# Performance work log

Hardware: AMD Instinct MI355X
Metric: run time of the kernel (lower is better)

## Reference

```python
import jax, jax.numpy as jnp
import numpy as np

H = 16
D_MODEL = 1024
D_K = D_MODEL // H
B, S = 4, 2048


def setup_inputs() -> dict:
    key = jax.random.key(0)
    ks = jax.random.split(key, 12)
    scale = 1.0 / np.sqrt(D_MODEL)
    inp = {
        "query": jax.random.normal(ks[0], (B, S, D_MODEL), jnp.float32),
        "key_in": jax.random.normal(ks[1], (B, S, D_MODEL), jnp.float32),
        "value": jax.random.normal(ks[2], (B, S, D_MODEL), jnp.float32),
        "mask": jax.random.randint(ks[3], (B, 1, S, S), 0, 2, jnp.int32),
    }
    # 4 Linear(d_model, d_model) layers: Wq, Wk, Wv, Wo (+ biases)
    names = ["q", "k", "v", "o"]
    for i, n in enumerate(names):
        inp[f"W{n}"] = jax.random.normal(ks[4 + i], (D_MODEL, D_MODEL), jnp.float32) * scale
        inp[f"b{n}"] = jax.random.normal(ks[8 + i], (D_MODEL,), jnp.float32) * scale
    return inp


def reference(query, key_in, value, mask, Wq, bq, Wk, bk, Wv, bv, Wo, bo):
    # Linear projections then split heads: [B,S,D] -> [B,H,S,Dk]
    def proj(x, W, b):
        y = jnp.einsum("bsd,ed->bse", x, W) + b  # torch Linear: x @ W.T + b
        return y.reshape(B, S, H, D_K).transpose(0, 2, 1, 3)

    q = proj(query, Wq, bq)
    k = proj(key_in, Wk, bk)
    v = proj(value, Wv, bv)

    scores = jnp.einsum("bhqd,bhkd->bhqk", q, k) / jnp.sqrt(jnp.float32(D_K))
    scores = jnp.where(mask == 0, jnp.float32(-1e9), scores)
    p_attn = jax.nn.softmax(scores, axis=-1)
    # dropout is identity in eval mode
    x = jnp.einsum("bhqk,bhkd->bhqd", p_attn, v)
    x = x.transpose(0, 2, 1, 3).reshape(B, S, D_MODEL)
    return jnp.einsum("bsd,ed->bse", x, Wo) + bo
```

## Files before the change

kernel.cpp:

```cpp
#include <hip/hip_runtime.h>
#include <hip/hip_bf16.h>

typedef __bf16 bf16_t;
typedef __attribute__((ext_vector_type(8))) __bf16 bf16x8;
typedef __attribute__((ext_vector_type(4))) __bf16 bf16x4;
typedef __attribute__((ext_vector_type(4))) float f32x4;

#define GAS __attribute__((address_space(1)))
#define LAS __attribute__((address_space(3)))

__device__ __forceinline__ void async_copy16(const bf16_t* g, bf16_t* l) {
    __builtin_amdgcn_global_load_lds((const GAS void*)g, (LAS void*)l, 16, 0, 0);
}

__global__ __launch_bounds__(256) void convert_kernel(
    const float* __restrict__ src, bf16_t* __restrict__ dst, int n)
{
    int i = (blockIdx.x * 256 + threadIdx.x) * 8;
    if (i >= n) return;
    f32x4 f0 = *(const f32x4*)(src + i);
    f32x4 f1 = *(const f32x4*)(src + i + 4);
    bf16x8 v;
#pragma unroll
    for (int j = 0; j < 4; j++) { v[j] = (bf16_t)f0[j]; v[4 + j] = (bf16_t)f1[j]; }
    *(bf16x8*)&dst[i] = v;
}

__global__ __launch_bounds__(256) void pack_mask_kernel(
    const int* __restrict__ mask, unsigned long long* __restrict__ out)
{
    int i = blockIdx.x * 256 + threadIdx.x;
    unsigned long long bits = __ballot(mask[i] != 0);
    if ((threadIdx.x & 63) == 0) out[i >> 6] = bits;
}

template<int MODE>
__global__ __launch_bounds__(256, 2) void gemm_nt(
    const bf16_t* __restrict__ A, const bf16_t* __restrict__ W,
    const float* __restrict__ bias, void* __restrict__ out_)
{
    __shared__ __align__(16) bf16_t Als[128 * 32];
    __shared__ __align__(16) bf16_t Bls[128 * 32];

    const int tid  = threadIdx.x;
    const int wave = tid >> 6, lane = tid & 63;
    const int quad = lane >> 4, lq = lane & 15;
    const int wm = wave >> 1, wn = wave & 1;
    const int tm = blockIdx.x * 128, tn = blockIdx.y * 128;
    const int K = 1024;

    const bf16_t* gA0 = A + (size_t)(tm + wave * 32 + (lane >> 2)) * K + (lane & 3) * 8;
    const bf16_t* gA1 = gA0 + (size_t)16 * K;
    const bf16_t* gB0 = W + (size_t)(tn + wave * 32 + (lane >> 2)) * K + (lane & 3) * 8;
    const bf16_t* gB1 = gB0 + (size_t)16 * K;
    bf16_t* lA0 = &Als[(wave * 32) * 32];
    bf16_t* lA1 = &Als[(wave * 32 + 16) * 32];
    bf16_t* lB0 = &Bls[(wave * 32) * 32];
    bf16_t* lB1 = &Bls[(wave * 32 + 16) * 32];

    f32x4 acc[4][4] = {};

    for (int k0 = 0; k0 < K; k0 += 32) {
        __syncthreads();
        async_copy16(gA0, lA0);
        async_copy16(gA1, lA1);
        async_copy16(gB0, lB0);
        async_copy16(gB1, lB1);
        gA0 += 32; gA1 += 32; gB0 += 32; gB1 += 32;
        __syncthreads();

        bf16x8 af[4], bfr[4];
#pragma unroll
        for (int i = 0; i < 4; i++) {
            af[i]  = *(const bf16x8*)&Als[(wm * 64 + i * 16 + lq) * 32 + quad * 8];
            bfr[i] = *(const bf16x8*)&Bls[(wn * 64 + i * 16 + lq) * 32 + quad * 8];
        }
#pragma unroll
        for (int i = 0; i < 4; i++)
#pragma unroll
            for (int j = 0; j < 4; j++) {
                if (MODE == 2)
                    acc[i][j] = __builtin_amdgcn_mfma_f32_16x16x32_bf16(bfr[j], af[i], acc[i][j], 0, 0, 0);
                else
                    acc[i][j] = __builtin_amdgcn_mfma_f32_16x16x32_bf16(af[i], bfr[j], acc[i][j], 0, 0, 0);
            }
    }

    float* outf = (float*)out_;
    bf16_t* outb = (bf16_t*)out_;
#pragma unroll
    for (int i = 0; i < 4; i++)
#pragma unroll
        for (int j = 0; j < 4; j++)
#pragma unroll
            for (int r = 0; r < 4; r++) {
                float v = acc[i][j][r];
                if (MODE == 0) {
                    int row = tm + wm * 64 + i * 16 + quad * 4 + r;
                    int col = tn + wn * 64 + j * 16 + lq;
                    outf[(size_t)row * 1024 + col] = v + bias[col];
                } else if (MODE == 1) {
                    int row = tm + wm * 64 + i * 16 + quad * 4 + r;
                    int col = tn + wn * 64 + j * 16 + lq;
                    v += bias[col];
                    int b = row >> 11, s = row & 2047;
                    int h = col >> 6,  dk = col & 63;
                    outb[(((size_t)(b * 16 + h) * 2048 + s) << 6) + dk] = (bf16_t)v;
                } else {
                    int n = tn + wn * 64 + j * 16 + quad * 4 + r;
                    int m = tm + wm * 64 + i * 16 + lq;
                    v += bias[n];
                    int b = m >> 11, s = m & 2047;
                    int h = n >> 6,  dk = n & 63;
                    outb[((size_t)((b * 16 + h) * 64 + dk) << 11) + s] = (bf16_t)v;
                }
            }
}

#define LDK 72
#define LDV 40
#define LDP 40

__global__ __launch_bounds__(256, 2) void attn_kernel(
    const bf16_t* __restrict__ Q, const bf16_t* __restrict__ Kh,
    const bf16_t* __restrict__ Vt, const unsigned int* __restrict__ mp,
    bf16_t* __restrict__ X)
{
    __shared__ __align__(16) bf16_t Kls[32 * LDK];
    __shared__ __align__(16) bf16_t Vls[64 * LDV];
    __shared__ __align__(16) bf16_t Pls[4][16 * LDP];

    const int tid  = threadIdx.x;
    const int wave = tid >> 6, lane = tid & 63;
    const int quad = lane >> 4, lq = lane & 15;
    const int bh = blockIdx.y;
    const int b  = bh >> 4;
    const int qw = blockIdx.x * 64 + wave * 16;

    const bf16_t* qptr = Q + ((size_t)bh * 2048 + qw + lq) * 64 + quad * 8;
    bf16x8 qf0 = *(const bf16x8*)qptr;
    bf16x8 qf1 = *(const bf16x8*)(qptr + 32);

    f32x4 o[4] = {};
    float lsum = 0.f;

    const int kr = tid >> 3, kc = tid & 7;
    const int vr = tid >> 2, vc = tid & 3;
    const bf16_t* gK = Kh + ((size_t)bh * 2048 + kr) * 64 + kc * 8;
    const bf16_t* gV = Vt + ((size_t)bh * 64 + vr) * 2048 + vc * 8;

    const unsigned int* mrow = mp + ((size_t)(b << 11) + qw + lq) * 64;

    for (int kt = 0; kt < 64; kt++) {
        unsigned int w = mrow[kt];
        bf16x8 kstage = *(const bf16x8*)gK;
        bf16x8 vstage = *(const bf16x8*)gV;
        gK += 2048; gV += 32;

        __syncthreads();
        *(bf16x8*)&Kls[kr * LDK + kc * 8] = kstage;
        *(bf16x8*)&Vls[vr * LDV + vc * 8] = vstage;
        __syncthreads();

        bf16_t* pb = &Pls[wave][0];
        const unsigned int wq = w >> (quad * 4);
#pragma unroll
        for (int nt = 0; nt < 2; nt++) {
            const bf16_t* krow = &Kls[(nt * 16 + lq) * LDK];
            bf16x8 kf0 = *(const bf16x8*)(krow + quad * 8);
            bf16x8 kf1 = *(const bf16x8*)(krow + 32 + quad * 8);
            f32x4 z = {};
            z = __builtin_amdgcn_mfma_f32_16x16x32_bf16(kf0, qf0, z, 0, 0, 0);
            z = __builtin_amdgcn_mfma_f32_16x16x32_bf16(kf1, qf1, z, 0, 0, 0);
            bf16x4 pk;
#pragma unroll
            for (int r = 0; r < 4; r++) {
                float sv = ((wq >> (nt * 16 + r)) & 1) ? z[r] * 0.125f : -1e9f;
                float p = __expf(sv);
                lsum += p;
                pk[r] = (bf16_t)p;
            }
            *(bf16x4*)&pb[lq * LDP + nt * 16 + quad * 4] = pk;
        }

        bf16x8 pf = *(const bf16x8*)&pb[lq * LDP + quad * 8];
#pragma unroll
        for (int dt = 0; dt < 4; dt++) {
            bf16x8 vf = *(const bf16x8*)&Vls[(dt * 16 + lq) * LDV + quad * 8];
            o[dt] = __builtin_amdgcn_mfma_f32_16x16x32_bf16(pf, vf, o[dt], 0, 0, 0);
        }
    }

    lsum += __shfl_xor(lsum, 16);
    lsum += __shfl_xor(lsum, 32);
    float rl[4];
#pragma unroll
    for (int r = 0; r < 4; r++) {
        float lv = __shfl(lsum, quad * 4 + r);
        rl[r] = (lv > 0.f) ? 1.0f / lv : 0.f;
    }
    const int h = bh & 15;
#pragma unroll
    for (int dt = 0; dt < 4; dt++)
#pragma unroll
        for (int r = 0; r < 4; r++) {
            int qrow = qw + quad * 4 + r;
            X[((size_t)(b * 2048) + qrow) * 1024 + h * 64 + dt * 16 + lq] =
                (bf16_t)(o[dt][r] * rl[r]);
        }
}

extern "C" void kernel_launch(void* const* d_in, const int* in_sizes, int n_in,
                              void* d_out, int out_size, void* d_ws, size_t ws_size,
                              hipStream_t stream)
{
    const float* query  = (const float*)d_in[0];
    const float* key_in = (const float*)d_in[1];
    const float* value  = (const float*)d_in[2];
    const int*   mask   = (const int*)d_in[3];

    char* ws = (char*)d_ws;
    const size_t SZ  = (size_t)8192 * 1024 * 2;
    const size_t MPK = (size_t)2 * 1024 * 1024;
    const size_t WSZ = (size_t)1024 * 1024 * 2;
    bf16_t* C   = (bf16_t*)(ws);
    bf16_t* Qb  = (bf16_t*)(ws + SZ);
    bf16_t* Kb  = (bf16_t*)(ws + 2 * SZ);
    bf16_t* Vtb = (bf16_t*)(ws + 3 * SZ);
    unsigned long long* mpack = (unsigned long long*)(ws + 4 * SZ);
    bf16_t* Wc[4];
    for (int i = 0; i < 4; i++)
        Wc[i] = (bf16_t*)(ws + 4 * SZ + MPK + i * WSZ);

    const size_t NEED = 4 * SZ + MPK + 4 * WSZ;
    if (ws_size < NEED) return;

    const int NACT = 8192 * 1024;
    for (int i = 0; i < 4; i++)
        convert_kernel<<<512, 256, 0, stream>>>((const float*)d_in[4 + 2 * i],
                                                Wc[i], 1024 * 1024);
    pack_mask_kernel<<<65536, 256, 0, stream>>>(mask, mpack);

    dim3 gg(64, 8);
    convert_kernel<<<4096, 256, 0, stream>>>(query, C, NACT);
    gemm_nt<1><<<gg, 256, 0, stream>>>(C, Wc[0], (const float*)d_in[5], Qb);
    convert_kernel<<<4096, 256, 0, stream>>>(key_in, C, NACT);
    gemm_nt<1><<<gg, 256, 0, stream>>>(C, Wc[1], (const float*)d_in[7], Kb);
    convert_kernel<<<4096, 256, 0, stream>>>(value, C, NACT);
    gemm_nt<2><<<gg, 256, 0, stream>>>(C, Wc[2], (const float*)d_in[9], Vtb);

    attn_kernel<<<dim3(32, 64), 256, 0, stream>>>(Qb, Kb, Vtb,
                                                  (const unsigned int*)mpack, C);
    gemm_nt<0><<<gg, 256, 0, stream>>>(C, Wc[3], (const float*)d_in[11], d_out);
}
```

Baseline: 473.7 us.

## Fuse activation conversion into QKV GEMM, double-buffer GEMMs and attention

The separate fp32-to-bf16 conversion passes for the activations are removed. The batched QKV GEMM (grid z=3) now loads fp32 A directly and converts it in registers, and the four weight conversions are merged into one launch. Both GEMMs and the attention kernel gain double-buffered LDS with a single barrier per step, so global loads overlap compute. Attention also gives each wave 32 query rows to reuse K/V tiles, at the cost of more registers and LDS.

Result: no change. 477.5 us (+0.8%).

```diff
diff --git a/kernel.cpp b/kernel.cpp
--- a/kernel.cpp
+++ b/kernel.cpp
@@ -13,17 +13,20 @@
     __builtin_amdgcn_global_load_lds((const GAS void*)g, (LAS void*)l, 16, 0, 0);
 }
 
-__global__ __launch_bounds__(256) void convert_kernel(
-    const float* __restrict__ src, bf16_t* __restrict__ dst, int n)
-{
-    int i = (blockIdx.x * 256 + threadIdx.x) * 8;
-    if (i >= n) return;
+__global__ __launch_bounds__(256) void wconvert_kernel(
+    const float* __restrict__ w0, const float* __restrict__ w1,
+    const float* __restrict__ w2, const float* __restrict__ w3,
+    bf16_t* __restrict__ dst)
+{
+    int which = blockIdx.x >> 9;
+    const float* src = which == 0 ? w0 : which == 1 ? w1 : which == 2 ? w2 : w3;
+    int i = ((blockIdx.x & 511) * 256 + threadIdx.x) * 8;
     f32x4 f0 = *(const f32x4*)(src + i);
     f32x4 f1 = *(const f32x4*)(src + i + 4);
     bf16x8 v;
 #pragma unroll
     for (int j = 0; j < 4; j++) { v[j] = (bf16_t)f0[j]; v[4 + j] = (bf16_t)f1[j]; }
-    *(bf16x8*)&dst[i] = v;
+    *(bf16x8*)&dst[(size_t)which * 1048576 + i] = v;
 }
 
 __global__ __launch_bounds__(256) void pack_mask_kernel(
@@ -34,13 +37,21 @@
     if ((threadIdx.x & 63) == 0) out[i >> 6] = bits;
 }
 
-template<int MODE>
-__global__ __launch_bounds__(256, 2) void gemm_nt(
-    const bf16_t* __restrict__ A, const bf16_t* __restrict__ W,
-    const float* __restrict__ bias, void* __restrict__ out_)
-{
-    __shared__ __align__(16) bf16_t Als[128 * 32];
-    __shared__ __align__(16) bf16_t Bls[128 * 32];
+__global__ __launch_bounds__(256, 2) void qkv_gemm(
+    const float* __restrict__ Aq, const float* __restrict__ Ak,
+    const float* __restrict__ Av, const bf16_t* __restrict__ Wall,
+    const float* __restrict__ bq, const float* __restrict__ bk,
+    const float* __restrict__ bv,
+    bf16_t* __restrict__ Qb, bf16_t* __restrict__ Kb, bf16_t* __restrict__ Vtb)
+{
+    const int z = blockIdx.z;
+    const float*  A    = z == 0 ? Aq : z == 1 ? Ak : Av;
+    const bf16_t* W    = Wall + (size_t)z * 1048576;
+    const float*  bias = z == 0 ? bq : z == 1 ? bk : bv;
+    bf16_t*       out  = z == 0 ? Qb : z == 1 ? Kb : Vtb;
+
+    __shared__ __align__(16) bf16_t Ab[2][128 * 32];
+    __shared__ __align__(16) bf16_t Wb[2][128 * 32];
 
     const int tid  = threadIdx.x;
     const int wave = tid >> 6, lane = tid & 63;
@@ -49,45 +60,57 @@
     const int tm = blockIdx.x * 128, tn = blockIdx.y * 128;
     const int K = 1024;
 
-    const bf16_t* gA0 = A + (size_t)(tm + wave * 32 + (lane >> 2)) * K + (lane & 3) * 8;
-    const bf16_t* gA1 = gA0 + (size_t)16 * K;
-    const bf16_t* gB0 = W + (size_t)(tn + wave * 32 + (lane >> 2)) * K + (lane & 3) * 8;
-    const bf16_t* gB1 = gB0 + (size_t)16 * K;
-    bf16_t* lA0 = &Als[(wave * 32) * 32];
-    bf16_t* lA1 = &Als[(wave * 32 + 16) * 32];
-    bf16_t* lB0 = &Bls[(wave * 32) * 32];
-    bf16_t* lB1 = &Bls[(wave * 32 + 16) * 32];
+    const int r0f = tid >> 3, c0f = tid & 7;
+    const float* gA = A + (size_t)(tm + r0f) * K + c0f * 4;
+    const bf16_t* gW0 = W + (size_t)(tn + wave * 32 + (lane >> 2)) * K + (lane & 3) * 8;
+    const bf16_t* gW1 = gW0 + (size_t)16 * K;
+    const int wd0 = (wave * 32) * 32, wd1 = (wave * 32 + 16) * 32;
+
+    f32x4 areg[4];
+#define LOAD_A(k) { _Pragma("unroll") \
+    for (int i = 0; i < 4; i++) areg[i] = *(const f32x4*)(gA + (size_t)(32 * i) * K + (k)); }
+#define WRITE_A(buf) { _Pragma("unroll") \
+    for (int i = 0; i < 4; i++) { bf16x4 v_; _Pragma("unroll") \
+        for (int j = 0; j < 4; j++) v_[j] = (bf16_t)areg[i][j]; \
+        *(bf16x4*)&Ab[buf][(r0f + 32 * i) * 32 + c0f * 4] = v_; } }
+#define DMA_W(k, buf) { async_copy16(gW0 + (k), &Wb[buf][wd0]); \
+                        async_copy16(gW1 + (k), &Wb[buf][wd1]); }
 
     f32x4 acc[4][4] = {};
 
-    for (int k0 = 0; k0 < K; k0 += 32) {
+    LOAD_A(0);
+    WRITE_A(0);
+    DMA_W(0, 0);
+    LOAD_A(32);
+    __syncthreads();
+
+    for (int t = 0; t < 32; ++t) {
+        if (t < 31) { WRITE_A((t + 1) & 1); DMA_W((t + 1) * 32, (t + 1) & 1); }
+        if (t < 30) { LOAD_A((t + 2) * 32); }
+
+        const int buf = t & 1;
+        bf16x8 af[4], bfr[4];
+#pragma unroll
+        for (int i = 0; i < 4; i++) {
+            af[i]  = *(const bf16x8*)&Ab[buf][(wm * 64 + i * 16 + lq) * 32 + quad * 8];
+            bfr[i] = *(const bf16x8*)&Wb[buf][(wn * 64 + i * 16 + lq) * 32 + quad * 8];
+        }
+        if (z == 2) {
+#pragma unroll
+            for (int i = 0; i < 4; i++)
+#pragma unroll
+                for (int j = 0; j < 4; j++)
+                    acc[i][j] = __builtin_amdgcn_mfma_f32_16x16x32_bf16(bfr[j], af[i], acc[i][j], 0, 0, 0);
+        } else {
+#pragma unroll
+            for (int i = 0; i < 4; i++)
+#pragma unroll
+                for (int j = 0; j < 4; j++)
+                    acc[i][j] = __builtin_amdgcn_mfma_f32_16x16x32_bf16(af[i], bfr[j], acc[i][j], 0, 0, 0);
+        }
         __syncthreads();
-        async_copy16(gA0, lA0);
-        async_copy16(gA1, lA1);
-        async_copy16(gB0, lB0);
-        async_copy16(gB1, lB1);
-        gA0 += 32; gA1 += 32; gB0 += 32; gB1 += 32;
-        __syncthreads();
-
-        bf16x8 af[4], bfr[4];
-#pragma unroll
-        for (int i = 0; i < 4; i++) {
-            af[i]  = *(const bf16x8*)&Als[(wm * 64 + i * 16 + lq) * 32 + quad * 8];
-            bfr[i] = *(const bf16x8*)&Bls[(wn * 64 + i * 16 + lq) * 32 + quad * 8];
-        }
-#pragma unroll
-        for (int i = 0; i < 4; i++)
-#pragma unroll
-            for (int j = 0; j < 4; j++) {
-                if (MODE == 2)
-                    acc[i][j] = __builtin_amdgcn_mfma_f32_16x16x32_bf16(bfr[j], af[i], acc[i][j], 0, 0, 0);
-                else
-                    acc[i][j] = __builtin_amdgcn_mfma_f32_16x16x32_bf16(af[i], bfr[j], acc[i][j], 0, 0, 0);
-            }
-    }
-
-    float* outf = (float*)out_;
-    bf16_t* outb = (bf16_t*)out_;
+    }
+
 #pragma unroll
     for (int i = 0; i < 4; i++)
 #pragma unroll
@@ -95,26 +118,86 @@
 #pragma unroll
             for (int r = 0; r < 4; r++) {
                 float v = acc[i][j][r];
-                if (MODE == 0) {
-                    int row = tm + wm * 64 + i * 16 + quad * 4 + r;
-                    int col = tn + wn * 64 + j * 16 + lq;
-                    outf[(size_t)row * 1024 + col] = v + bias[col];
-                } else if (MODE == 1) {
+                if (z <= 1) {
                     int row = tm + wm * 64 + i * 16 + quad * 4 + r;
                     int col = tn + wn * 64 + j * 16 + lq;
                     v += bias[col];
                     int b = row >> 11, s = row & 2047;
                     int h = col >> 6,  dk = col & 63;
-                    outb[(((size_t)(b * 16 + h) * 2048 + s) << 6) + dk] = (bf16_t)v;
+                    out[(((size_t)(b * 16 + h) * 2048 + s) << 6) + dk] = (bf16_t)v;
                 } else {
                     int n = tn + wn * 64 + j * 16 + quad * 4 + r;
                     int m = tm + wm * 64 + i * 16 + lq;
                     v += bias[n];
                     int b = m >> 11, s = m & 2047;
                     int h = n >> 6,  dk = n & 63;
-                    outb[((size_t)((b * 16 + h) * 64 + dk) << 11) + s] = (bf16_t)v;
+                    out[((size_t)((b * 16 + h) * 64 + dk) << 11) + s] = (bf16_t)v;
                 }
             }
+#undef LOAD_A
+#undef WRITE_A
+#undef DMA_W
+}
+
+__global__ __launch_bounds__(256, 2) void gemm_o(
+    const bf16_t* __restrict__ A, const bf16_t* __restrict__ W,
+    const float* __restrict__ bias, float* __restrict__ out)
+{
+    __shared__ __align__(16) bf16_t Ab[2][128 * 32];
+    __shared__ __align__(16) bf16_t Wb[2][128 * 32];
+
+    const int tid  = threadIdx.x;
+    const int wave = tid >> 6, lane = tid & 63;
+    const int quad = lane >> 4, lq = lane & 15;
+    const int wm = wave >> 1, wn = wave & 1;
+    const int tm = blockIdx.x * 128, tn = blockIdx.y * 128;
+    const int K = 1024;
+
+    const bf16_t* gA0 = A + (size_t)(tm + wave * 32 + (lane >> 2)) * K + (lane & 3) * 8;
+    const bf16_t* gA1 = gA0 + (size_t)16 * K;
+    const bf16_t* gW0 = W + (size_t)(tn + wave * 32 + (lane >> 2)) * K + (lane & 3) * 8;
+    const bf16_t* gW1 = gW0 + (size_t)16 * K;
+    const int d0 = (wave * 32) * 32, d1 = (wave * 32 + 16) * 32;
+
+#define DMA_T(k, buf) { async_copy16(gA0 + (k), &Ab[buf][d0]); \
+                        async_copy16(gA1 + (k), &Ab[buf][d1]); \
+                        async_copy16(gW0 + (k), &Wb[buf][d0]); \
+                        async_copy16(gW1 + (k), &Wb[buf][d1]); }
+
+    f32x4 acc[4][4] = {};
+
+    DMA_T(0, 0);
+    __syncthreads();
+
+    for (int t = 0; t < 32; ++t) {
+        if (t < 31) DMA_T((t + 1) * 32, (t + 1) & 1);
+
+        const int buf = t & 1;
+        bf16x8 af[4], bfr[4];
+#pragma unroll
+        for (int i = 0; i < 4; i++) {
+            af[i]  = *(const bf16x8*)&Ab[buf][(wm * 64 + i * 16 + lq) * 32 + quad * 8];
+            bfr[i] = *(const bf16x8*)&Wb[buf][(wn * 64 + i * 16 + lq) * 32 + quad * 8];
+        }
+#pragma unroll
+        for (int i = 0; i < 4; i++)
+#pragma unroll
+            for (int j = 0; j < 4; j++)
+                acc[i][j] = __builtin_amdgcn_mfma_f32_16x16x32_bf16(af[i], bfr[j], acc[i][j], 0, 0, 0);
+        __syncthreads();
+    }
+
+#pragma unroll
+    for (int i = 0; i < 4; i++)
+#pragma unroll
+        for (int j = 0; j < 4; j++)
+#pragma unroll
+            for (int r = 0; r < 4; r++) {
+                int row = tm + wm * 64 + i * 16 + quad * 4 + r;
+                int col = tn + wn * 64 + j * 16 + lq;
+                out[(size_t)row * 1024 + col] = acc[i][j][r] + bias[col];
+            }
+#undef DMA_T
 }
 
 #define LDK 72
@@ -126,88 +209,116 @@
     const bf16_t* __restrict__ Vt, const unsigned int* __restrict__ mp,
     bf16_t* __restrict__ X)
 {
-    __shared__ __align__(16) bf16_t Kls[32 * LDK];
-    __shared__ __align__(16) bf16_t Vls[64 * LDV];
-    __shared__ __align__(16) bf16_t Pls[4][16 * LDP];
+    __shared__ __align__(16) bf16_t KbL[2][32 * LDK];
+    __shared__ __align__(16) bf16_t VbL[2][64 * LDV];
+    __shared__ __align__(16) bf16_t Pls[4][32 * LDP];
 
     const int tid  = threadIdx.x;
     const int wave = tid >> 6, lane = tid & 63;
     const int quad = lane >> 4, lq = lane & 15;
-    const int bh = blockIdx.y;
-    const int b  = bh >> 4;
-    const int qw = blockIdx.x * 64 + wave * 16;
-
-    const bf16_t* qptr = Q + ((size_t)bh * 2048 + qw + lq) * 64 + quad * 8;
-    bf16x8 qf0 = *(const bf16x8*)qptr;
-    bf16x8 qf1 = *(const bf16x8*)(qptr + 32);
-
-    f32x4 o[4] = {};
-    float lsum = 0.f;
+    const int bh = blockIdx.y, b = bh >> 4, h = bh & 15;
+    const int qw = blockIdx.x * 128 + wave * 32;
+
+    bf16x8 qf[2][2];
+#pragma unroll
+    for (int s = 0; s < 2; s++) {
+        const bf16_t* qptr = Q + ((size_t)bh * 2048 + qw + s * 16 + lq) * 64 + quad * 8;
+        qf[s][0] = *(const bf16x8*)qptr;
+        qf[s][1] = *(const bf16x8*)(qptr + 32);
+    }
+
+    f32x4 o[2][4] = {};
+    float lsum[2] = {0.f, 0.f};
 
     const int kr = tid >> 3, kc = tid & 7;
     const int vr = tid >> 2, vc = tid & 3;
     const bf16_t* gK = Kh + ((size_t)bh * 2048 + kr) * 64 + kc * 8;
     const bf16_t* gV = Vt + ((size_t)bh * 64 + vr) * 2048 + vc * 8;
-
-    const unsigned int* mrow = mp + ((size_t)(b << 11) + qw + lq) * 64;
-
-    for (int kt = 0; kt < 64; kt++) {
-        unsigned int w = mrow[kt];
-        bf16x8 kstage = *(const bf16x8*)gK;
-        bf16x8 vstage = *(const bf16x8*)gV;
-        gK += 2048; gV += 32;
-
+    const unsigned int* mrow0 = mp + ((size_t)(b << 11) + qw + lq) * 64;
+    const unsigned int* mrow1 = mrow0 + 16 * 64;
+
+    bf16x8 kst = *(const bf16x8*)gK;
+    bf16x8 vst = *(const bf16x8*)gV;
+    *(bf16x8*)&KbL[0][kr * LDK + kc * 8] = kst;
+    *(bf16x8*)&VbL[0][vr * LDV + vc * 8] = vst;
+    kst = *(const bf16x8*)(gK + 2048);
+    vst = *(const bf16x8*)(gV + 32);
+    unsigned int mw0 = mrow0[0], mw1 = mrow1[0];
+    __syncthreads();
+
+    for (int t = 0; t < 64; ++t) {
+        if (t < 63) {
+            *(bf16x8*)&KbL[(t + 1) & 1][kr * LDK + kc * 8] = kst;
+            *(bf16x8*)&VbL[(t + 1) & 1][vr * LDV + vc * 8] = vst;
+        }
+        if (t < 62) {
+            kst = *(const bf16x8*)(gK + (size_t)(t + 2) * 2048);
+            vst = *(const bf16x8*)(gV + (size_t)(t + 2) * 32);
+        }
+        unsigned int w0 = mw0, w1 = mw1;
+        if (t < 63) { mw0 = mrow0[t + 1]; mw1 = mrow1[t + 1]; }
+
+        const bf16_t* Kc = &KbL[t & 1][0];
+        const bf16_t* Vc = &VbL[t & 1][0];
+        bf16_t* pb = &Pls[wave][0];
+
+        bf16x8 kf[2][2];
+#pragma unroll
+        for (int nt = 0; nt < 2; nt++) {
+            kf[nt][0] = *(const bf16x8*)&Kc[(nt * 16 + lq) * LDK + quad * 8];
+            kf[nt][1] = *(const bf16x8*)&Kc[(nt * 16 + lq) * LDK + 32 + quad * 8];
+        }
+#pragma unroll
+        for (int s = 0; s < 2; s++) {
+            const unsigned int wq = (s ? w1 : w0) >> (quad * 4);
+#pragma unroll
+            for (int nt = 0; nt < 2; nt++) {
+                f32x4 z = {};
+                z = __builtin_amdgcn_mfma_f32_16x16x32_bf16(kf[nt][0], qf[s][0], z, 0, 0, 0);
+                z = __builtin_amdgcn_mfma_f32_16x16x32_bf16(kf[nt][1], qf[s][1], z, 0, 0, 0);
+                bf16x4 pk;
+#pragma unroll
+                for (int r = 0; r < 4; r++) {
+                    float sv = ((wq >> (nt * 16 + r)) & 1) ? z[r] * 0.125f : -1e9f;
+                    float p = __expf(sv);
+                    lsum[s] += p;
+                    pk[r] = (bf16_t)p;
+                }
+                *(bf16x4*)&pb[(s * 16 + lq) * LDP + nt * 16 + quad * 4] = pk;
+            }
+        }
+
+        bf16x8 vf[4];
+#pragma unroll
+        for (int dt = 0; dt < 4; dt++)
+            vf[dt] = *(const bf16x8*)&Vc[(dt * 16 + lq) * LDV + quad * 8];
+#pragma unroll
+        for (int s = 0; s < 2; s++) {
+            bf16x8 pf = *(const bf16x8*)&pb[(s * 16 + lq) * LDP + quad * 8];
+#pragma unroll
+            for (int dt = 0; dt < 4; dt++)
+                o[s][dt] = __builtin_amdgcn_mfma_f32_16x16x32_bf16(pf, vf[dt], o[s][dt], 0, 0, 0);
+        }
         __syncthreads();
-        *(bf16x8*)&Kls[kr * LDK + kc * 8] = kstage;
-        *(bf16x8*)&Vls[vr * LDV + vc * 8] = vstage;
-        __syncthreads();
-
-        bf16_t* pb = &Pls[wave][0];
-        const unsigned int wq = w >> (quad * 4);
-#pragma unroll
-        for (int nt = 0; nt < 2; nt++) {
-            const bf16_t* krow = &Kls[(nt * 16 + lq) * LDK];
-            bf16x8 kf0 = *(const bf16x8*)(krow + quad * 8);
-            bf16x8 kf1 = *(const bf16x8*)(krow + 32 + quad * 8);
-            f32x4 z = {};
-            z = __builtin_amdgcn_mfma_f32_16x16x32_bf16(kf0, qf0, z, 0, 0, 0);
-            z = __builtin_amdgcn_mfma_f32_16x16x32_bf16(kf1, qf1, z, 0, 0, 0);
-            bf16x4 pk;
+    }
+
+#pragma unroll
+    for (int s = 0; s < 2; s++) {
+        lsum[s] += __shfl_xor(lsum[s], 16);
+        lsum[s] += __shfl_xor(lsum[s], 32);
+    }
+#pragma unroll
+    for (int s = 0; s < 2; s++)
+#pragma unroll
+        for (int dt = 0; dt < 4; dt++)
 #pragma unroll
             for (int r = 0; r < 4; r++) {
-                float sv = ((wq >> (nt * 16 + r)) & 1) ? z[r] * 0.125f : -1e9f;
-                float p = __expf(sv);
-                lsum += p;
-                pk[r] = (bf16_t)p;
+                float lv = __shfl(lsum[s], quad * 4 + r);
+                float rl = (lv > 0.f) ? 1.0f / lv : 0.f;
+                int qrow = qw + s * 16 + quad * 4 + r;
+                X[((size_t)(b * 2048) + qrow) * 1024 + h * 64 + dt * 16 + lq] =
+                    (bf16_t)(o[s][dt][r] * rl);
             }
-            *(bf16x4*)&pb[lq * LDP + nt * 16 + quad * 4] = pk;
-        }
-
-        bf16x8 pf = *(const bf16x8*)&pb[lq * LDP + quad * 8];
-#pragma unroll
-        for (int dt = 0; dt < 4; dt++) {
-            bf16x8 vf = *(const bf16x8*)&Vls[(dt * 16 + lq) * LDV + quad * 8];
-            o[dt] = __builtin_amdgcn_mfma_f32_16x16x32_bf16(pf, vf, o[dt], 0, 0, 0);
-        }
-    }
-
-    lsum += __shfl_xor(lsum, 16);
-    lsum += __shfl_xor(lsum, 32);
-    float rl[4];
-#pragma unroll
-    for (int r = 0; r < 4; r++) {
-        float lv = __shfl(lsum, quad * 4 + r);
-        rl[r] = (lv > 0.f) ? 1.0f / lv : 0.f;
-    }
-    const int h = bh & 15;
-#pragma unroll
-    for (int dt = 0; dt < 4; dt++)
-#pragma unroll
-        for (int r = 0; r < 4; r++) {
-            int qrow = qw + quad * 4 + r;
-            X[((size_t)(b * 2048) + qrow) * 1024 + h * 64 + dt * 16 + lq] =
-                (bf16_t)(o[dt][r] * rl[r]);
-        }
 }
 
 extern "C" void kernel_launch(void* const* d_in, const int* in_sizes, int n_in,
@@ -222,34 +333,29 @@
     char* ws = (char*)d_ws;
     const size_t SZ  = (size_t)8192 * 1024 * 2;
     const size_t MPK = (size_t)2 * 1024 * 1024;
-    const size_t WSZ = (size_t)1024 * 1024 * 2;
-    bf16_t* C   = (bf16_t*)(ws);
-    bf16_t* Qb  = (bf16_t*)(ws + SZ);
-    bf16_t* Kb  = (bf16_t*)(ws + 2 * SZ);
-    bf16_t* Vtb = (bf16_t*)(ws + 3 * SZ);
+    bf16_t* Qb  = (bf16_t*)(ws);
+    bf16_t* Kb  = (bf16_t*)(ws + SZ);
+    bf16_t* Vtb = (bf16_t*)(ws + 2 * SZ);
+    bf16_t* Xb  = (bf16_t*)(ws + 3 * SZ);
     unsigned long long* mpack = (unsigned long long*)(ws + 4 * SZ);
-    bf16_t* Wc[4];
-    for (int i = 0; i < 4; i++)
-        Wc[i] = (bf16_t*)(ws + 4 * SZ + MPK + i * WSZ);
-
-    const size_t NEED = 4 * SZ + MPK + 4 * WSZ;
+    bf16_t* Wc = (bf16_t*)(ws + 4 * SZ + MPK);
+
+    const size_t NEED = 4 * SZ + MPK + (size_t)4 * 1048576 * 2;
     if (ws_size < NEED) return;
 
-    const int NACT = 8192 * 1024;
-    for (int i = 0; i < 4; i++)
-        convert_kernel<<<512, 256, 0, stream>>>((const float*)d_in[4 + 2 * i],
-                                                Wc[i], 1024 * 1024);
+    wconvert_kernel<<<2048, 256, 0, stream>>>(
+        (const float*)d_in[4], (const float*)d_in[6],
+        (const float*)d_in[8], (const float*)d_in[10], Wc);
     pack_mask_kernel<<<65536, 256, 0, stream>>>(mask, mpack);
 
-    dim3 gg(64, 8);
-    convert_kernel<<<4096, 256, 0, stream>>>(query, C, NACT);
-    gemm_nt<1><<<gg, 256, 0, stream>>>(C, Wc[0], (const float*)d_in[5], Qb);
-    convert_kernel<<<4096, 256, 0, stream>>>(key_in, C, NACT);
-    gemm_nt<1><<<gg, 256, 0, stream>>>(C, Wc[1], (const float*)d_in[7], Kb);
-    convert_kernel<<<4096, 256, 0, stream>>>(value, C, NACT);
-    gemm_nt<2><<<gg, 256, 0, stream>>>(C, Wc[2], (const float*)d_in[9], Vtb);
-
-    attn_kernel<<<dim3(32, 64), 256, 0, stream>>>(Qb, Kb, Vtb,
-                                                  (const unsigned int*)mpack, C);
-    gemm_nt<0><<<gg, 256, 0, stream>>>(C, Wc[3], (const float*)d_in[11], d_out);
-}
+    qkv_gemm<<<dim3(64, 8, 3), 256, 0, stream>>>(
+        query, key_in, value, Wc,
+        (const float*)d_in[5], (const float*)d_in[7], (const float*)d_in[9],
+        Qb, Kb, Vtb);
+
+    attn_kernel<<<dim3(16, 64), 256, 0, stream>>>(Qb, Kb, Vtb,
+                                                  (const unsigned int*)mpack, Xb);
+
+    gemm_o<<<dim3(64, 8), 256, 0, stream>>>(Xb, Wc + (size_t)3 * 1048576,
+                                            (const float*)d_in[11], (float*)d_out);
+}
```
